# Optimization experiments

Measured on AMD Instinct MI355X. Metric: run time of the kernel, lower is better.

The kernel has to match this reference:

```python
import jax, jax.numpy as jnp
import numpy as np

K = 3          # kernel_size (cubic)
S = 1          # stride
N_ITER = 3     # routing_iter
LAMBDA = 0.01  # inverse temperature used in M-step (CapsLayer default)
EPS = 1e-9


def _space_to_batch(x, k, s):
    # x: [B, D, H, W, C, ...] -> [B, oD, oH, oW, k^3 * C, ...]
    # patch ordering (kd, kh, kw, c) matches CapsLayer's gather+transpose+reshape.
    B, D, H, W, C = x.shape[:5]
    trail = x.shape[5:]
    oD = (D - k) // s + 1
    oH = (H - k) // s + 1
    oW = (W - k) // s + 1
    blocks = []
    for kd in range(k):
        for kh in range(k):
            for kw in range(k):
                blocks.append(x[:, kd:kd + oD * s:s, kh:kh + oH * s:s, kw:kw + oW * s:s])
    p = jnp.stack(blocks, axis=4)  # [B,oD,oH,oW,k^3,C,...]
    return p.reshape((B, oD, oH, oW, k ** 3 * C) + trail)


def _lse(x, axis):
    return jax.scipy.special.logsumexp(x, axis=axis, keepdims=True)


def _m_step(log_R, log_act, vote, bv, ba):
    # log_R: [...,I,O,1], log_act: [...,I,1,1], vote: [...,I,O,P]
    log_Ra = log_R + log_act
    R_sum = jnp.sum(jnp.exp(log_Ra), axis=-3, keepdims=True)        # [...,1,O,1]
    log_nR = log_Ra - _lse(log_Ra, axis=-3)                          # [...,I,O,1]
    pose = jnp.sum(vote * jnp.exp(log_nR), axis=-3, keepdims=True)   # [...,1,O,P]
    log_var = _lse(log_nR + jnp.log(jnp.square(vote - pose) + EPS), axis=-3)
    cost = R_sum * (bv + 0.5 * log_var)                              # [...,1,O,P]
    logit = LAMBDA * (ba - jnp.sum(cost, axis=-1, keepdims=True))    # [...,1,O,1]
    return pose, log_var, jax.nn.log_sigmoid(logit)


def _e_step(pose, log_var, log_act_out, vote):
    # per-dim Gaussian log-likelihood of votes under (pose, var)
    lp = -0.5 * (jnp.square(vote - pose) / jnp.exp(log_var) + log_var + jnp.log(2.0 * jnp.pi))
    lp = jnp.sum(lp, axis=-1, keepdims=True)                         # [...,I,O,1]
    logit = log_act_out + lp
    return logit - _lse(logit, axis=-2)                              # softmax over O


def _forward(pose, activation, W, beta_v, beta_a):
    pb = _space_to_batch(pose, K, S)            # [B,oD,oH,oW,I,4,4]
    ab = _space_to_batch(activation, K, S)      # [B,oD,oH,oW,I]
    # votes: W[i,o] @ pose_patch[...,i] -> [B,oD,oH,oW,I,O,4,4]
    vote = jnp.einsum('iork,bdhwikc->bdhwiorc', W, pb)
    vs = vote.shape
    vote = vote.reshape(vs[:-2] + (vs[-2] * vs[-1],))   # [...,I,O,16]
    nO = vote.shape[-2]
    log_act = jnp.log(ab + EPS)[..., None, None]        # [...,I,1,1]
    log_R = jnp.full(vote.shape[:-1] + (1,), -jnp.log(float(nO)), vote.dtype)
    bv = beta_v[None, None, None, None, None, :, :]     # [1,1,1,1,1,O,1]
    ba = beta_a[None, None, None, None, None, :, :]
    for t in range(N_ITER):
        v = vote if t == N_ITER - 1 else jax.lax.stop_gradient(vote)
        p, log_var, log_a = _m_step(log_R, log_act, v, bv, ba)
        if t < N_ITER - 1:
            log_R = _e_step(p, log_var, log_a, jax.lax.stop_gradient(vote))
    out_pose = jnp.squeeze(p, axis=-3).reshape(vs[:4] + (vs[-3], vs[-2], vs[-1]))  # [B,oD,oH,oW,O,4,4]
    out_act = jnp.exp(jnp.squeeze(log_a, axis=(-3, -1)))                            # [B,oD,oH,oW,O]
    return out_pose, out_act


def setup_inputs() -> dict:
    key = jax.random.key(0)
    k1, k2, k3, k4, k5 = jax.random.split(key, 5)
    pose = jax.random.normal(k1, (1, 12, 12, 12, 8, 4, 4), dtype=jnp.float32)
    activation = jax.random.uniform(k2, (1, 12, 12, 12, 8), dtype=jnp.float32)
    W = jax.random.normal(k3, (216, 16, 4, 4), dtype=jnp.float32)
    beta_v = jax.random.normal(k4, (16, 1), dtype=jnp.float32)
    beta_a = jax.random.normal(k5, (16, 1), dtype=jnp.float32)
    return {"pose": pose, "activation": activation, "W": W, "beta_v": beta_v, "beta_a": beta_a}


def reference(pose, activation, W, beta_v, beta_a):
    return _forward(pose, activation, W, beta_v, beta_a)
```

## Files before the change

### kernel.cpp

```cpp
#include <hip/hip_runtime.h>

#define NITER 3
#define LAMBDA 0.01f
#define EPS 1e-9f
#define LOG2PI 1.8378770664093453f

#define DIN 12
#define CIN 8
#define NI 216
#define NO 16
#define PPAD 20
#define RSTR 216

__global__ __launch_bounds__(512) __attribute__((amdgpu_waves_per_eu(2, 2)))
void caps_em_kernel(const float* __restrict__ pose,
                    const float* __restrict__ act,
                    const float* __restrict__ W,
                    const float* __restrict__ beta_v,
                    const float* __restrict__ beta_a,
                    float* __restrict__ out)
{
    __shared__ __align__(16) float sPT[NI][PPAD];
    __shared__ __align__(16) float sRaT[NO][RSTR];
    __shared__ float sAct[NI];
    __shared__ __align__(16) float sPoseM[NO][16];
    __shared__ __align__(16) float sIvM[NO][16];
    __shared__ float sCo[NO];

    const int t = threadIdx.x;
    const int b = blockIdx.x;
    const int od = b / 100;
    const int rem = b - od * 100;
    const int oh = rem / 10;
    const int ow = rem - oh * 10;

    const int o = t >> 5;
    const int j = t & 31;

    const float4* W4 = (const float4*)W;
    float4 w[7][4];
#pragma unroll
    for (int k = 0; k < 7; ++k) {
        const int iw = min(j + 32 * k, NI - 1);
        const float4* Wp = W4 + (iw * 16 + o) * 4;
        w[k][0] = Wp[0];
        w[k][1] = Wp[1];
        w[k][2] = Wp[2];
        w[k][3] = Wp[3];
    }

    for (int u = t; u < NI * 4; u += 512) {
        int i = u >> 2, q = u & 3;
        int ci = i & 7, n = i >> 3;
        int kw = n % 3, n2 = n / 3;
        int kh = n2 % 3, kd = n2 / 3;
        const float4 v = *(const float4*)&pose[((((od + kd) * DIN + (oh + kh)) * DIN + (ow + kw)) * CIN + ci) * 16 + q * 4];
        sPT[i][0 + q]  = v.x;
        sPT[i][4 + q]  = v.y;
        sPT[i][8 + q]  = v.z;
        sPT[i][12 + q] = v.w;
    }
    if (t < NI) {
        int i = t;
        int ci = i & 7, n = i >> 3;
        int kw = n % 3, n2 = n / 3;
        int kh = n2 % 3, kd = n2 / 3;
        sAct[i] = act[(((od + kd) * DIN + (oh + kh)) * DIN + (ow + kw)) * CIN + ci] + EPS;
    }
    const float bv_o = beta_v[o];
    const float ba_o = beta_a[o];
    __syncthreads();

    float vo[7][16];
#pragma unroll
    for (int k = 0; k < 7; ++k) {
        const int ip = min(j + 32 * k, NI - 1);
#pragma unroll
        for (int cc = 0; cc < 4; ++cc) {
            const float4 pt = *(const float4*)&sPT[ip][cc * 4];
#pragma unroll
            for (int rr = 0; rr < 4; ++rr) {
                float v = w[k][rr].x * pt.x;
                v = fmaf(w[k][rr].y, pt.y, v);
                v = fmaf(w[k][rr].z, pt.z, v);
                v = fmaf(w[k][rr].w, pt.w, v);
                vo[k][rr * 4 + cc] = v;
            }
        }
    }

    const int b4 = (j >> 4) & 1, b3 = (j >> 3) & 1, b2 = (j >> 2) & 1, b1 = (j >> 1) & 1;
    const bool lastPartial = (j >= 24);

    for (int it = 0; it < NITER; ++it) {
        float m1[16], m2[16];
#pragma unroll
        for (int q = 0; q < 16; ++q) { m1[q] = 0.f; m2[q] = 0.f; }
        float rs = 0.f;
#pragma unroll
        for (int k = 0; k < 7; ++k) {
            const int ip = min(j + 32 * k, NI - 1);
            float ra = (it == 0) ? sAct[ip] * 0.0625f : sRaT[o][ip];
            if (k == 6 && lastPartial) ra = 0.f;
            rs += ra;
#pragma unroll
            for (int q = 0; q < 16; ++q) {
                const float v  = vo[k][q];
                const float rv = ra * v;
                m1[q] += rv;
                m2[q] = fmaf(rv, v, m2[q]);
            }
        }

#pragma unroll
        for (int q = 0; q < 8; ++q) {
            float s1 = b4 ? m1[q] : m1[q + 8];
            float s2 = b4 ? m2[q] : m2[q + 8];
            m1[q] = (b4 ? m1[q + 8] : m1[q]) + __shfl_xor(s1, 16);
            m2[q] = (b4 ? m2[q + 8] : m2[q]) + __shfl_xor(s2, 16);
        }
#pragma unroll
        for (int q = 0; q < 4; ++q) {
            float s1 = b3 ? m1[q] : m1[q + 4];
            float s2 = b3 ? m2[q] : m2[q + 4];
            m1[q] = (b3 ? m1[q + 4] : m1[q]) + __shfl_xor(s1, 8);
            m2[q] = (b3 ? m2[q + 4] : m2[q]) + __shfl_xor(s2, 8);
        }
#pragma unroll
        for (int q = 0; q < 2; ++q) {
            float s1 = b2 ? m1[q] : m1[q + 2];
            float s2 = b2 ? m2[q] : m2[q + 2];
            m1[q] = (b2 ? m1[q + 2] : m1[q]) + __shfl_xor(s1, 4);
            m2[q] = (b2 ? m2[q + 2] : m2[q]) + __shfl_xor(s2, 4);
        }
        {
            float s1 = b1 ? m1[0] : m1[1];
            float s2 = b1 ? m2[0] : m2[1];
            m1[0] = (b1 ? m1[1] : m1[0]) + __shfl_xor(s1, 2);
            m2[0] = (b1 ? m2[1] : m2[0]) + __shfl_xor(s2, 2);
        }
        m1[0] += __shfl_xor(m1[0], 1);
        m2[0] += __shfl_xor(m2[0], 1);
        rs += __shfl_xor(rs, 16);
        rs += __shfl_xor(rs, 8);
        rs += __shfl_xor(rs, 4);
        rs += __shfl_xor(rs, 2);
        rs += __shfl_xor(rs, 1);
        const int e = j >> 1;

        const float inv_rs = 1.0f / rs;
        const float pe = m1[0] * inv_rs;
        const float ve = fmaxf(m2[0] * inv_rs - pe * pe, 0.0f) + EPS;
        const float lv = __logf(ve);

        float SL = lv;
        SL += __shfl_xor(SL, 1);
        SL += __shfl_xor(SL, 2);
        SL += __shfl_xor(SL, 4);
        SL += __shfl_xor(SL, 8);
        SL += __shfl_xor(SL, 16);
        SL *= 0.5f;

        const float cost  = rs * (16.0f * bv_o + 0.5f * SL);
        const float logit = LAMBDA * (ba_o - cost);

        if (it == NITER - 1) {
            if ((j & 1) == 0) out[(b * NO + o) * 16 + e] = pe;
            if (j == 0) out[256000 + b * NO + o] = 1.0f / (1.0f + __expf(-logit));
            return;
        }

        const float log_a = (logit >= 0.0f) ? -log1pf(__expf(-logit))
                                            : logit - log1pf(__expf(logit));
        if ((j & 1) == 0) {
            sPoseM[o][e] = pe;
            sIvM[o][e]   = 1.0f / ve;
        }
        if (j == 0) sCo[o] = log_a - 0.5f * SL - 8.0f * LOG2PI;
        __syncthreads();

        {
            float pv[16], iv16[16];
            *(float4*)&pv[0]    = *(const float4*)&sPoseM[o][0];
            *(float4*)&pv[4]    = *(const float4*)&sPoseM[o][4];
            *(float4*)&pv[8]    = *(const float4*)&sPoseM[o][8];
            *(float4*)&pv[12]   = *(const float4*)&sPoseM[o][12];
            *(float4*)&iv16[0]  = *(const float4*)&sIvM[o][0];
            *(float4*)&iv16[4]  = *(const float4*)&sIvM[o][4];
            *(float4*)&iv16[8]  = *(const float4*)&sIvM[o][8];
            *(float4*)&iv16[12] = *(const float4*)&sIvM[o][12];
            const float Co = sCo[o];
#pragma unroll
            for (int k = 0; k < 7; ++k) {
                const int i = j + 32 * k;
                float q = 0.f;
#pragma unroll
                for (int qq = 0; qq < 16; ++qq) {
                    const float d = vo[k][qq] - pv[qq];
                    q = fmaf(d * d, iv16[qq], q);
                }
                if (!(k == 6 && lastPartial)) {
                    sRaT[o][i] = Co - 0.5f * q;
                }
            }
        }
        __syncthreads();

        if (t < NI) {
            float l[16];
            float mx = -1e30f;
#pragma unroll
            for (int oo = 0; oo < 16; ++oo) { l[oo] = sRaT[oo][t]; mx = fmaxf(mx, l[oo]); }
            float s = 0.f;
#pragma unroll
            for (int oo = 0; oo < 16; ++oo) { l[oo] = __expf(l[oo] - mx); s += l[oo]; }
            const float sc = sAct[t] / s;
#pragma unroll
            for (int oo = 0; oo < 16; ++oo) sRaT[oo][t] = sc * l[oo];
        }
        __syncthreads();
    }
}

extern "C" void kernel_launch(void* const* d_in, const int* in_sizes, int n_in,
                              void* d_out, int out_size, void* d_ws, size_t ws_size,
                              hipStream_t stream) {
    const float* pose = (const float*)d_in[0];
    const float* actv = (const float*)d_in[1];
    const float* W    = (const float*)d_in[2];
    const float* bv   = (const float*)d_in[3];
    const float* ba   = (const float*)d_in[4];
    float* out = (float*)d_out;
    caps_em_kernel<<<dim3(1000), dim3(512), 0, stream>>>(pose, actv, W, bv, ba, out);
}
```

Baseline: 131.9 us.

## Split each output capsule's input votes across 64 lanes with 1024-thread blocks

Doubles the block to 1024 threads so each output capsule gets a full 64-lane wavefront. Each lane now holds 4 rather than 7 vote groups, which cuts per-thread register use for votes and weights and lets the kernel target 4 waves per EU. The shuffle reduction tree gains a level to match. The softmax over output capsules is spread across 4 threads per input with shuffle reductions instead of 1 thread per input. The shared routing array's row stride is padded from 216 to 220 to reduce LDS bank conflicts, at the cost of more shuffles and a larger block that must fit on one CU.

After: 149.7 us. 13.5% more time.

```diff
diff --git a/kernel.cpp b/kernel.cpp
--- a/kernel.cpp
+++ b/kernel.cpp
@@ -10,9 +10,9 @@
 #define NI 216
 #define NO 16
 #define PPAD 20
-#define RSTR 216
-
-__global__ __launch_bounds__(512) __attribute__((amdgpu_waves_per_eu(2, 2)))
+#define RSTR 220
+
+__global__ __launch_bounds__(1024) __attribute__((amdgpu_waves_per_eu(4, 4)))
 void caps_em_kernel(const float* __restrict__ pose,
                     const float* __restrict__ act,
                     const float* __restrict__ W,
@@ -34,14 +34,14 @@
     const int oh = rem / 10;
     const int ow = rem - oh * 10;
 
-    const int o = t >> 5;
-    const int j = t & 31;
+    const int o = t >> 6;
+    const int j = t & 63;
 
     const float4* W4 = (const float4*)W;
-    float4 w[7][4];
-#pragma unroll
-    for (int k = 0; k < 7; ++k) {
-        const int iw = min(j + 32 * k, NI - 1);
+    float4 w[4][4];
+#pragma unroll
+    for (int k = 0; k < 4; ++k) {
+        const int iw = min(j + 64 * k, NI - 1);
         const float4* Wp = W4 + (iw * 16 + o) * 4;
         w[k][0] = Wp[0];
         w[k][1] = Wp[1];
@@ -49,8 +49,8 @@
         w[k][3] = Wp[3];
     }
 
-    for (int u = t; u < NI * 4; u += 512) {
-        int i = u >> 2, q = u & 3;
+    if (t < NI * 4) {
+        int i = t >> 2, q = t & 3;
         int ci = i & 7, n = i >> 3;
         int kw = n % 3, n2 = n / 3;
         int kh = n2 % 3, kd = n2 / 3;
@@ -71,10 +71,10 @@
     const float ba_o = beta_a[o];
     __syncthreads();
 
-    float vo[7][16];
-#pragma unroll
-    for (int k = 0; k < 7; ++k) {
-        const int ip = min(j + 32 * k, NI - 1);
+    float vo[4][16];
+#pragma unroll
+    for (int k = 0; k < 4; ++k) {
+        const int ip = min(j + 64 * k, NI - 1);
 #pragma unroll
         for (int cc = 0; cc < 4; ++cc) {
             const float4 pt = *(const float4*)&sPT[ip][cc * 4];
@@ -89,7 +89,7 @@
         }
     }
 
-    const int b4 = (j >> 4) & 1, b3 = (j >> 3) & 1, b2 = (j >> 2) & 1, b1 = (j >> 1) & 1;
+    const int b5 = (j >> 5) & 1, b4 = (j >> 4) & 1, b3 = (j >> 3) & 1, b2 = (j >> 2) & 1;
     const bool lastPartial = (j >= 24);
 
     for (int it = 0; it < NITER; ++it) {
@@ -98,10 +98,10 @@
         for (int q = 0; q < 16; ++q) { m1[q] = 0.f; m2[q] = 0.f; }
         float rs = 0.f;
 #pragma unroll
-        for (int k = 0; k < 7; ++k) {
-            const int ip = min(j + 32 * k, NI - 1);
+        for (int k = 0; k < 4; ++k) {
+            const int ip = min(j + 64 * k, NI - 1);
             float ra = (it == 0) ? sAct[ip] * 0.0625f : sRaT[o][ip];
-            if (k == 6 && lastPartial) ra = 0.f;
+            if (k == 3 && lastPartial) ra = 0.f;
             rs += ra;
 #pragma unroll
             for (int q = 0; q < 16; ++q) {
@@ -114,39 +114,42 @@
 
 #pragma unroll
         for (int q = 0; q < 8; ++q) {
-            float s1 = b4 ? m1[q] : m1[q + 8];
-            float s2 = b4 ? m2[q] : m2[q + 8];
-            m1[q] = (b4 ? m1[q + 8] : m1[q]) + __shfl_xor(s1, 16);
-            m2[q] = (b4 ? m2[q + 8] : m2[q]) + __shfl_xor(s2, 16);
+            float s1 = b5 ? m1[q] : m1[q + 8];
+            float s2 = b5 ? m2[q] : m2[q + 8];
+            m1[q] = (b5 ? m1[q + 8] : m1[q]) + __shfl_xor(s1, 32);
+            m2[q] = (b5 ? m2[q + 8] : m2[q]) + __shfl_xor(s2, 32);
         }
 #pragma unroll
         for (int q = 0; q < 4; ++q) {
-            float s1 = b3 ? m1[q] : m1[q + 4];
-            float s2 = b3 ? m2[q] : m2[q + 4];
-            m1[q] = (b3 ? m1[q + 4] : m1[q]) + __shfl_xor(s1, 8);
-            m2[q] = (b3 ? m2[q + 4] : m2[q]) + __shfl_xor(s2, 8);
+            float s1 = b4 ? m1[q] : m1[q + 4];
+            float s2 = b4 ? m2[q] : m2[q + 4];
+            m1[q] = (b4 ? m1[q + 4] : m1[q]) + __shfl_xor(s1, 16);
+            m2[q] = (b4 ? m2[q + 4] : m2[q]) + __shfl_xor(s2, 16);
         }
 #pragma unroll
         for (int q = 0; q < 2; ++q) {
-            float s1 = b2 ? m1[q] : m1[q + 2];
-            float s2 = b2 ? m2[q] : m2[q + 2];
-            m1[q] = (b2 ? m1[q + 2] : m1[q]) + __shfl_xor(s1, 4);
-            m2[q] = (b2 ? m2[q + 2] : m2[q]) + __shfl_xor(s2, 4);
+            float s1 = b3 ? m1[q] : m1[q + 2];
+            float s2 = b3 ? m2[q] : m2[q + 2];
+            m1[q] = (b3 ? m1[q + 2] : m1[q]) + __shfl_xor(s1, 8);
+            m2[q] = (b3 ? m2[q + 2] : m2[q]) + __shfl_xor(s2, 8);
         }
         {
-            float s1 = b1 ? m1[0] : m1[1];
-            float s2 = b1 ? m2[0] : m2[1];
-            m1[0] = (b1 ? m1[1] : m1[0]) + __shfl_xor(s1, 2);
-            m2[0] = (b1 ? m2[1] : m2[0]) + __shfl_xor(s2, 2);
-        }
+            float s1 = b2 ? m1[0] : m1[1];
+            float s2 = b2 ? m2[0] : m2[1];
+            m1[0] = (b2 ? m1[1] : m1[0]) + __shfl_xor(s1, 4);
+            m2[0] = (b2 ? m2[1] : m2[0]) + __shfl_xor(s2, 4);
+        }
+        m1[0] += __shfl_xor(m1[0], 2);
+        m2[0] += __shfl_xor(m2[0], 2);
         m1[0] += __shfl_xor(m1[0], 1);
         m2[0] += __shfl_xor(m2[0], 1);
+        rs += __shfl_xor(rs, 32);
         rs += __shfl_xor(rs, 16);
         rs += __shfl_xor(rs, 8);
         rs += __shfl_xor(rs, 4);
         rs += __shfl_xor(rs, 2);
         rs += __shfl_xor(rs, 1);
-        const int e = j >> 1;
+        const int e = j >> 2;
 
         const float inv_rs = 1.0f / rs;
         const float pe = m1[0] * inv_rs;
@@ -159,20 +162,21 @@
         SL += __shfl_xor(SL, 4);
         SL += __shfl_xor(SL, 8);
         SL += __shfl_xor(SL, 16);
-        SL *= 0.5f;
+        SL += __shfl_xor(SL, 32);
+        SL *= 0.25f;
 
         const float cost  = rs * (16.0f * bv_o + 0.5f * SL);
         const float logit = LAMBDA * (ba_o - cost);
 
         if (it == NITER - 1) {
-            if ((j & 1) == 0) out[(b * NO + o) * 16 + e] = pe;
+            if ((j & 3) == 0) out[(b * NO + o) * 16 + e] = pe;
             if (j == 0) out[256000 + b * NO + o] = 1.0f / (1.0f + __expf(-logit));
             return;
         }
 
         const float log_a = (logit >= 0.0f) ? -log1pf(__expf(-logit))
                                             : logit - log1pf(__expf(logit));
-        if ((j & 1) == 0) {
+        if ((j & 3) == 0) {
             sPoseM[o][e] = pe;
             sIvM[o][e]   = 1.0f / ve;
         }
@@ -191,32 +195,37 @@
             *(float4*)&iv16[12] = *(const float4*)&sIvM[o][12];
             const float Co = sCo[o];
 #pragma unroll
-            for (int k = 0; k < 7; ++k) {
-                const int i = j + 32 * k;
+            for (int k = 0; k < 4; ++k) {
+                const int i = j + 64 * k;
                 float q = 0.f;
 #pragma unroll
                 for (int qq = 0; qq < 16; ++qq) {
                     const float d = vo[k][qq] - pv[qq];
                     q = fmaf(d * d, iv16[qq], q);
                 }
-                if (!(k == 6 && lastPartial)) {
+                if (!(k == 3 && lastPartial)) {
                     sRaT[o][i] = Co - 0.5f * q;
                 }
             }
         }
         __syncthreads();
 
-        if (t < NI) {
-            float l[16];
+        if (t < NI * 4) {
+            const int i = t >> 2, p = t & 3;
+            float l[4];
             float mx = -1e30f;
 #pragma unroll
-            for (int oo = 0; oo < 16; ++oo) { l[oo] = sRaT[oo][t]; mx = fmaxf(mx, l[oo]); }
+            for (int q = 0; q < 4; ++q) { l[q] = sRaT[p * 4 + q][i]; mx = fmaxf(mx, l[q]); }
+            mx = fmaxf(mx, __shfl_xor(mx, 1));
+            mx = fmaxf(mx, __shfl_xor(mx, 2));
             float s = 0.f;
 #pragma unroll
-            for (int oo = 0; oo < 16; ++oo) { l[oo] = __expf(l[oo] - mx); s += l[oo]; }
-            const float sc = sAct[t] / s;
-#pragma unroll
-            for (int oo = 0; oo < 16; ++oo) sRaT[oo][t] = sc * l[oo];
+            for (int q = 0; q < 4; ++q) { l[q] = __expf(l[q] - mx); s += l[q]; }
+            s += __shfl_xor(s, 1);
+            s += __shfl_xor(s, 2);
+            const float sc = sAct[i] / s;
+#pragma unroll
+            for (int q = 0; q < 4; ++q) sRaT[p * 4 + q][i] = sc * l[q];
         }
         __syncthreads();
     }
@@ -231,5 +240,5 @@
     const float* bv   = (const float*)d_in[3];
     const float* ba   = (const float*)d_in[4];
     float* out = (float*)d_out;
-    caps_em_kernel<<<dim3(1000), dim3(512), 0, stream>>>(pose, actv, W, bv, ba, out);
+    caps_em_kernel<<<dim3(1000), dim3(1024), 0, stream>>>(pose, actv, W, bv, ba, out);
 }
```
